# Performance work log

Measured on AMD Instinct MI355X. Metric: run time of the kernel, lower is better.

## Reference

```python
import jax, jax.numpy as jnp
import numpy as np

T, B, E, H = 1024, 2, 1024, 16
D = E // H


def setup_inputs() -> dict:
    key = jax.random.key(0)
    ks = jax.random.split(key, 5)
    s = 1.0 / np.sqrt(E)  # xavier_uniform bound ~ sqrt(6/(fan_in+fan_out)); scale suffices for a numeric baseline
    return {
        "query": jax.random.normal(ks[0], (T, B, E), jnp.float32),
        "key_": jax.random.normal(ks[1], (T, B, E), jnp.float32),
        "value": jax.random.normal(ks[2], (T, B, E), jnp.float32),
        "in_proj_weight": jax.random.uniform(ks[3], (3 * E, E), jnp.float32, -s, s),
        "in_proj_bias": jnp.zeros((3 * E,), jnp.float32),
        "out_proj_weight": jax.random.uniform(ks[4], (E, E), jnp.float32, -s, s),
        "out_proj_bias": jnp.zeros((E,), jnp.float32),
    }


def reference(query, key_, value, in_proj_weight, in_proj_bias, out_proj_weight, out_proj_bias):
    # Faithful to CumulativeLinearMultiheadAttentionKV.forward with
    # batch_first=False, is_causal=True, no padding mask, no kv cache.
    Tl, Bl, El = query.shape
    wq, wk, wv = jnp.split(in_proj_weight, 3, axis=0)
    bq, bk, bv = jnp.split(in_proj_bias, 3)
    q = query @ wq.T + bq          # (T, B, E)
    k = key_ @ wk.T + bk
    v = value @ wv.T + bv

    def to_bhtd(x):
        return x.reshape(Tl, Bl, H, D).transpose(1, 2, 0, 3)  # (B, H, T, D)

    q, k, v = to_bhtd(q), to_bhtd(k), to_bhtd(v)

    scale = 1.0 / np.sqrt(D)  # SDPA-style default scale (scale=None)
    # cumulative linear attention: prefix sums of k_s \otimes v_s
    kv = jnp.einsum('bhsk,bhsv->bhskv', k, v)        # (B, H, T, D, D)
    kv_store = jnp.cumsum(kv, axis=2)                # causal KV state per step
    out = jnp.einsum('bhtk,bhtkv->bhtv', q, kv_store) * scale  # (B, H, T, D)

    out = out.transpose(2, 0, 1, 3).reshape(Tl, Bl, El)  # back to (T, B, E)
    out = out @ out_proj_weight.T + out_proj_bias
    return out
```

## Files before the change

kernel.cpp:

```cpp
#include <hip/hip_runtime.h>


#define E_DIM 1024

typedef short bf16x8 __attribute__((ext_vector_type(8)));
typedef float f32x4  __attribute__((ext_vector_type(4)));

__device__ inline unsigned short f2bf(float f) {
    unsigned u = __builtin_bit_cast(unsigned, f);
    u = (u + 0x7FFFu + ((u >> 16) & 1u)) >> 16;
    return (unsigned short)u;
}

__device__ inline void gload_lds16(const void* g, void* l) {
    __builtin_amdgcn_global_load_lds(
        (const __attribute__((address_space(1))) unsigned int*)g,
        (__attribute__((address_space(3))) unsigned int*)l, 16, 0, 0);
}

__device__ inline int swzb(int row, int colbyte) {
    return colbyte ^ ((row & 7) << 4);
}

__global__ __launch_bounds__(256) void k_castw(
    const float* __restrict__ w_in, const float* __restrict__ w_out,
    unsigned short* __restrict__ dst)
{
    const int id8 = blockIdx.x * 256 + threadIdx.x;
    const int WI8 = 3 * E_DIM * E_DIM / 8;
    const float* src = (id8 < WI8) ? (w_in + (size_t)id8 * 8)
                                   : (w_out + (size_t)(id8 - WI8) * 8);
    float4 f0 = *reinterpret_cast<const float4*>(src);
    float4 f1 = *reinterpret_cast<const float4*>(src + 4);
    ushort4 o0, o1;
    o0.x = f2bf(f0.x); o0.y = f2bf(f0.y); o0.z = f2bf(f0.z); o0.w = f2bf(f0.w);
    o1.x = f2bf(f1.x); o1.y = f2bf(f1.y); o1.z = f2bf(f1.z); o1.w = f2bf(f1.w);
    *reinterpret_cast<ushort4*>(dst + (size_t)id8 * 8)     = o0;
    *reinterpret_cast<ushort4*>(dst + (size_t)id8 * 8 + 4) = o1;
}

__global__ __launch_bounds__(256) void k_gin(
    const float* __restrict__ q_in, const float* __restrict__ k_in,
    const float* __restrict__ v_in, const unsigned short* __restrict__ Wibf,
    const float* __restrict__ b_in,
    unsigned short* __restrict__ qslab, unsigned short* __restrict__ kslab,
    unsigned short* __restrict__ vtb)
{
    const int i = blockIdx.x;
    const int tile = (i & 7) * 48 + (i >> 3);
    const int z = tile >> 7;
    const int rem = tile & 127;
    const int x = rem >> 5, y = rem & 31;

    const float* X = (z == 0) ? q_in : (z == 1 ? k_in : v_in);
    const unsigned short* W = Wibf + (size_t)z * 1048576;
    const float* bz = b_in + z * E_DIM;

    const int nBase = x * 256;
    const int mBase = y * 64;
    const int b = mBase >> 10, tBase = mBase & 1023;

    __shared__ short As[2][64 * 64];
    __shared__ short Bs[2][256 * 64];

    const int tid = threadIdx.x;
    const int lane = tid & 63, wave = tid >> 6;
    const int wr = wave >> 1, wc = wave & 1;
    const int l15 = lane & 15, l4 = lane >> 4;

    auto stage = [&](int bufI, int k0) {
        #pragma unroll
        for (int l = 0; l < 8; ++l) {
            int off = l * 4096 + tid * 16;
            int row = off >> 7, cb = off & 127;
            gload_lds16((const char*)W + ((size_t)(nBase + row) * E_DIM + k0) * 2
                            + swzb(row, cb),
                        (char*)&Bs[bufI][0] + off);
        }
        #pragma unroll
        for (int l = 0; l < 2; ++l) {
            int u = tid + 256 * l;
            int row = u >> 3, cslot = u & 7;
            const float* src = &X[(size_t)((tBase + row) * 2 + b) * E_DIM
                                  + k0 + cslot * 8];
            float4 f0 = *reinterpret_cast<const float4*>(src);
            float4 f1 = *reinterpret_cast<const float4*>(src + 4);
            bf16x8 p;
            p[0] = (short)f2bf(f0.x); p[1] = (short)f2bf(f0.y);
            p[2] = (short)f2bf(f0.z); p[3] = (short)f2bf(f0.w);
            p[4] = (short)f2bf(f1.x); p[5] = (short)f2bf(f1.y);
            p[6] = (short)f2bf(f1.z); p[7] = (short)f2bf(f1.w);
            *reinterpret_cast<bf16x8*>(
                &As[bufI][row * 64 + (swzb(row, cslot * 16) >> 1)]) = p;
        }
    };

    f32x4 acc[2][8] = {};

    stage(0, 0);
    __syncthreads();
    int cur = 0;
    for (int it = 0; it < 16; ++it) {
        if (it < 15) stage(cur ^ 1, (it + 1) * 64);
        #pragma unroll
        for (int kk = 0; kk < 64; kk += 32) {
            bf16x8 af[2], bfr[8];
            #pragma unroll
            for (int ii = 0; ii < 2; ++ii) {
                int row = wr * 32 + ii * 16 + l15;
                af[ii] = *reinterpret_cast<const bf16x8*>(
                    &As[cur][row * 64 + (swzb(row, (kk + l4 * 8) * 2) >> 1)]);
            }
            #pragma unroll
            for (int j = 0; j < 8; ++j) {
                int row = wc * 128 + j * 16 + l15;
                bfr[j] = *reinterpret_cast<const bf16x8*>(
                    &Bs[cur][row * 64 + (swzb(row, (kk + l4 * 8) * 2) >> 1)]);
            }
            #pragma unroll
            for (int ii = 0; ii < 2; ++ii)
                #pragma unroll
                for (int j = 0; j < 8; ++j)
                    acc[ii][j] = __builtin_amdgcn_mfma_f32_16x16x32_bf16(
                        af[ii], bfr[j], acc[ii][j], 0, 0, 0);
        }
        __syncthreads();
        cur ^= 1;
    }

    #pragma unroll
    for (int ii = 0; ii < 2; ++ii) {
        int t0 = tBase + wr * 32 + ii * 16 + l4 * 4;
        #pragma unroll
        for (int j = 0; j < 8; ++j) {
            int col = nBase + wc * 128 + j * 16 + l15;
            float bv = bz[col];
            unsigned short v4[4];
            #pragma unroll
            for (int q = 0; q < 4; ++q) v4[q] = f2bf(acc[ii][j][q] + bv);
            if (z == 0) {
                #pragma unroll
                for (int q = 0; q < 4; ++q)
                    qslab[(size_t)b * 1048576 + (size_t)(t0 + q) * E_DIM + col] = v4[q];
            } else if (z == 1) {
                #pragma unroll
                for (int q = 0; q < 4; ++q)
                    kslab[(size_t)b * 1048576 + (size_t)(t0 + q) * E_DIM + col] = v4[q];
            } else {
                ushort4 w = {v4[0], v4[1], v4[2], v4[3]};
                *reinterpret_cast<ushort4*>(
                    &vtb[((size_t)b * 1024 + col) * 1024 + t0]) = w;
            }
        }
    }
}

__global__ __launch_bounds__(256) void k_attn(
    const unsigned short* __restrict__ qslab, const unsigned short* __restrict__ kslab,
    const unsigned short* __restrict__ vtb, unsigned short* __restrict__ attnbf)
{
    const int i = blockIdx.x;
    const int xcd = i & 7, u = i >> 3;
    const int bh = xcd * 4 + (u >> 4);
    const int qtr = u & 15;
    const int qt = ((u >> 5) & 1) ? (15 - qtr) : qtr;
    const int b = bh >> 4, h = bh & 15;
    const int colb = h * 64, t0q = qt * 64;

    __shared__ short Qs[64 * 64];
    __shared__ short Ks[2][64 * 64];
    __shared__ short Vts[2][64 * 64];
    __shared__ short Ss[64 * 72];

    const int tid = threadIdx.x;
    const int lane = tid & 63, wave = tid >> 6;
    const int wr = wave >> 1, wc = wave & 1;
    const int l15 = lane & 15, l4 = lane >> 4;

    auto stageKV = [&](int bufI, int c) {
        int t0k = c * 64;
        #pragma unroll
        for (int l = 0; l < 2; ++l) {
            int off = l * 4096 + tid * 16;
            int row = off >> 7, cb = off & 127;
            int scb = swzb(row, cb);
            gload_lds16((const char*)kslab +
                            ((size_t)b * 1048576 + (size_t)(t0k + row) * E_DIM + colb) * 2 + scb,
                        (char*)&Ks[bufI][0] + off);
            gload_lds16((const char*)vtb +
                            (((size_t)(b * 1024 + colb + row)) * 1024 + t0k) * 2 + scb,
                        (char*)&Vts[bufI][0] + off);
        }
    };

    #pragma unroll
    for (int l = 0; l < 2; ++l) {
        int off = l * 4096 + tid * 16;
        int row = off >> 7, cb = off & 127;
        gload_lds16((const char*)qslab +
                        ((size_t)b * 1048576 + (size_t)(t0q + row) * E_DIM + colb) * 2
                        + swzb(row, cb),
                    (char*)Qs + off);
    }
    stageKV(0, 0);
    __syncthreads();

    f32x4 oacc[2][2] = {};
    int cur = 0;

    for (int c = 0; c <= qt; ++c) {
        if (c < qt) stageKV(cur ^ 1, c + 1);

        f32x4 sacc[2][2] = {};
        #pragma unroll
        for (int kk = 0; kk < 64; kk += 32) {
            bf16x8 af[2], bfr[2];
            #pragma unroll
            for (int ii = 0; ii < 2; ++ii) {
                int row = wr * 32 + ii * 16 + l15;
                af[ii] = *reinterpret_cast<const bf16x8*>(
                    &Qs[row * 64 + (swzb(row, (kk + l4 * 8) * 2) >> 1)]);
            }
            #pragma unroll
            for (int j = 0; j < 2; ++j) {
                int row = wc * 32 + j * 16 + l15;
                bfr[j] = *reinterpret_cast<const bf16x8*>(
                    &Ks[cur][row * 64 + (swzb(row, (kk + l4 * 8) * 2) >> 1)]);
            }
            #pragma unroll
            for (int ii = 0; ii < 2; ++ii)
                #pragma unroll
                for (int j = 0; j < 2; ++j)
                    sacc[ii][j] = __builtin_amdgcn_mfma_f32_16x16x32_bf16(
                        af[ii], bfr[j], sacc[ii][j], 0, 0, 0);
        }
        const bool diag = (c == qt);
        #pragma unroll
        for (int ii = 0; ii < 2; ++ii) {
            #pragma unroll
            for (int j = 0; j < 2; ++j) {
                int kr = wc * 32 + j * 16 + l15;
                #pragma unroll
                for (int q = 0; q < 4; ++q) {
                    int qr = wr * 32 + ii * 16 + l4 * 4 + q;
                    short sv = (short)f2bf(sacc[ii][j][q]);
                    Ss[qr * 72 + kr] = (!diag || kr <= qr) ? sv : (short)0;
                }
            }
        }
        __syncthreads();

        #pragma unroll
        for (int kk = 0; kk < 64; kk += 32) {
            bf16x8 af[2], bfr[2];
            #pragma unroll
            for (int ii = 0; ii < 2; ++ii)
                af[ii] = *reinterpret_cast<const bf16x8*>(
                            &Ss[(wr * 32 + ii * 16 + l15) * 72 + kk + l4 * 8]);
            #pragma unroll
            for (int j = 0; j < 2; ++j) {
                int row = wc * 32 + j * 16 + l15;
                bfr[j] = *reinterpret_cast<const bf16x8*>(
                    &Vts[cur][row * 64 + (swzb(row, (kk + l4 * 8) * 2) >> 1)]);
            }
            #pragma unroll
            for (int ii = 0; ii < 2; ++ii)
                #pragma unroll
                for (int j = 0; j < 2; ++j)
                    oacc[ii][j] = __builtin_amdgcn_mfma_f32_16x16x32_bf16(
                        af[ii], bfr[j], oacc[ii][j], 0, 0, 0);
        }
        __syncthreads();
        cur ^= 1;
    }

    #pragma unroll
    for (int ii = 0; ii < 2; ++ii) {
        #pragma unroll
        for (int j = 0; j < 2; ++j) {
            int dv = wc * 32 + j * 16 + l15;
            #pragma unroll
            for (int q = 0; q < 4; ++q) {
                int qr = wr * 32 + ii * 16 + l4 * 4 + q;
                attnbf[(size_t)b * 1048576 + (size_t)(t0q + qr) * E_DIM + colb + dv] =
                    f2bf(oacc[ii][j][q] * 0.125f);
            }
        }
    }
}

__global__ __launch_bounds__(256) void k_gout(
    const unsigned short* __restrict__ attnbf, const unsigned short* __restrict__ Wobf,
    const float* __restrict__ bias, float* __restrict__ out)
{
    const int i = blockIdx.x;
    const int tile = (i & 7) * 64 + (i >> 3);
    const int x = tile & 15, y = tile >> 4;
    const int nBase = x * 64;
    const int mBase = y * 64;

    __shared__ short As[2][64 * 64];
    __shared__ short Bs[2][64 * 64];

    const int tid = threadIdx.x;
    const int lane = tid & 63, wave = tid >> 6;
    const int wr = wave >> 1, wc = wave & 1;
    const int l15 = lane & 15, l4 = lane >> 4;

    auto stage = [&](int bufI, int k0) {
        #pragma unroll
        for (int l = 0; l < 2; ++l) {
            int off = l * 4096 + tid * 16;
            int row = off >> 7, cb = off & 127;
            int scb = swzb(row, cb);
            gload_lds16((const char*)Wobf + ((size_t)(nBase + row) * E_DIM + k0) * 2 + scb,
                        (char*)&Bs[bufI][0] + off);
            int r = mBase + row, t = r >> 1, bb = r & 1;
            gload_lds16((const char*)attnbf +
                            ((size_t)bb * 1048576 + (size_t)t * E_DIM + k0) * 2 + scb,
                        (char*)&As[bufI][0] + off);
        }
    };

    f32x4 acc[2][2] = {};

    stage(0, 0);
    __syncthreads();
    int cur = 0;
    for (int it = 0; it < 16; ++it) {
        if (it < 15) stage(cur ^ 1, (it + 1) * 64);
        #pragma unroll
        for (int kk = 0; kk < 64; kk += 32) {
            bf16x8 af[2], bfr[2];
            #pragma unroll
            for (int ii = 0; ii < 2; ++ii) {
                int row = wr * 32 + ii * 16 + l15;
                af[ii] = *reinterpret_cast<const bf16x8*>(
                    &As[cur][row * 64 + (swzb(row, (kk + l4 * 8) * 2) >> 1)]);
            }
            #pragma unroll
            for (int j = 0; j < 2; ++j) {
                int row = wc * 32 + j * 16 + l15;
                bfr[j] = *reinterpret_cast<const bf16x8*>(
                    &Bs[cur][row * 64 + (swzb(row, (kk + l4 * 8) * 2) >> 1)]);
            }
            #pragma unroll
            for (int ii = 0; ii < 2; ++ii)
                #pragma unroll
                for (int j = 0; j < 2; ++j)
                    acc[ii][j] = __builtin_amdgcn_mfma_f32_16x16x32_bf16(
                        af[ii], bfr[j], acc[ii][j], 0, 0, 0);
        }
        __syncthreads();
        cur ^= 1;
    }

    #pragma unroll
    for (int ii = 0; ii < 2; ++ii) {
        int r0 = mBase + wr * 32 + ii * 16 + l4 * 4;
        #pragma unroll
        for (int j = 0; j < 2; ++j) {
            int col = nBase + wc * 32 + j * 16 + l15;
            float bv = bias[col];
            #pragma unroll
            for (int q = 0; q < 4; ++q)
                out[(size_t)(r0 + q) * E_DIM + col] = acc[ii][j][q] + bv;
        }
    }
}

extern "C" void kernel_launch(void* const* d_in, const int* in_sizes, int n_in,
                              void* d_out, int out_size, void* d_ws, size_t ws_size,
                              hipStream_t stream)
{
    const float* q_in  = (const float*)d_in[0];
    const float* k_in  = (const float*)d_in[1];
    const float* v_in  = (const float*)d_in[2];
    const float* w_in  = (const float*)d_in[3];
    const float* b_in  = (const float*)d_in[4];
    const float* w_out = (const float*)d_in[5];
    const float* b_out = (const float*)d_in[6];

    char* w = (char*)d_ws;
    unsigned short* Wibf   = (unsigned short*)w;
    unsigned short* Wobf   = (unsigned short*)(w + 6291456);
    unsigned short* qslab  = (unsigned short*)(w + 8388608);
    unsigned short* kslab  = (unsigned short*)(w + 12582912);
    unsigned short* vtb    = (unsigned short*)(w + 16777216);
    unsigned short* attnbf = (unsigned short*)(w + 20971520);
    float* outp = (float*)d_out;

    k_castw<<<2048, 256, 0, stream>>>(w_in, w_out, Wibf);
    k_gin<<<384, 256, 0, stream>>>(q_in, k_in, v_in, Wibf, b_in, qslab, kslab, vtb);
    k_attn<<<512, 256, 0, stream>>>(qslab, kslab, vtb, attnbf);
    k_gout<<<512, 256, 0, stream>>>(attnbf, Wobf, b_out, outp);
}
```

Baseline: 155.5 us.

## Accumulate K^T V prefix state for off-diagonal chunks instead of per-chunk QK^T

The attention kernel now builds a per-block prefix state P = sum over earlier chunks of K^T V, using a transposed K copy written by the input projection. It applies Q·P once and computes the masked QK^T·V only for the diagonal chunk. This removes the per-chunk S writes to LDS, the extra barrier and the second MFMA pass from the off-diagonal loop. In exchange, the projection writes an extra transposed K buffer, PTs adds LDS use, and P is rounded to bf16 before the final product, which may shift accuracy.

```diff
diff --git a/kernel.cpp b/kernel.cpp
--- a/kernel.cpp
+++ b/kernel.cpp
@@ -44,7 +44,7 @@
     const float* __restrict__ v_in, const unsigned short* __restrict__ Wibf,
     const float* __restrict__ b_in,
     unsigned short* __restrict__ qslab, unsigned short* __restrict__ kslab,
-    unsigned short* __restrict__ vtb)
+    unsigned short* __restrict__ ktb,   unsigned short* __restrict__ vtb)
 {
     const int i = blockIdx.x;
     const int tile = (i & 7) * 48 + (i >> 3);
@@ -146,6 +146,9 @@
                 #pragma unroll
                 for (int q = 0; q < 4; ++q)
                     kslab[(size_t)b * 1048576 + (size_t)(t0 + q) * E_DIM + col] = v4[q];
+                ushort4 w = {v4[0], v4[1], v4[2], v4[3]};
+                *reinterpret_cast<ushort4*>(
+                    &ktb[((size_t)b * 1024 + col) * 1024 + t0]) = w;
             } else {
                 ushort4 w = {v4[0], v4[1], v4[2], v4[3]};
                 *reinterpret_cast<ushort4*>(
@@ -157,7 +160,8 @@
 
 __global__ __launch_bounds__(256) void k_attn(
     const unsigned short* __restrict__ qslab, const unsigned short* __restrict__ kslab,
-    const unsigned short* __restrict__ vtb, unsigned short* __restrict__ attnbf)
+    const unsigned short* __restrict__ ktb,  const unsigned short* __restrict__ vtb,
+    unsigned short* __restrict__ attnbf)
 {
     const int i = blockIdx.x;
     const int xcd = i & 7, u = i >> 3;
@@ -168,28 +172,40 @@
     const int colb = h * 64, t0q = qt * 64;
 
     __shared__ short Qs[64 * 64];
-    __shared__ short Ks[2][64 * 64];
-    __shared__ short Vts[2][64 * 64];
+    __shared__ short KB[2][64 * 64];
+    __shared__ short VB[2][64 * 64];
     __shared__ short Ss[64 * 72];
+    __shared__ short PTs[64 * 72];
 
     const int tid = threadIdx.x;
     const int lane = tid & 63, wave = tid >> 6;
     const int wr = wave >> 1, wc = wave & 1;
     const int l15 = lane & 15, l4 = lane >> 4;
 
-    auto stageKV = [&](int bufI, int c) {
+    auto stageP = [&](int bufI, int c) {
         int t0k = c * 64;
+        #pragma unroll
+        for (int l = 0; l < 2; ++l) {
+            int off = l * 4096 + tid * 16;
+            int row = off >> 7, cb = off & 127;
+            int scb = swzb(row, cb);
+            size_t trn = ((size_t)(b * 1024 + colb + row)) * 1024 + t0k;
+            gload_lds16((const char*)ktb + trn * 2 + scb, (char*)&KB[bufI][0] + off);
+            gload_lds16((const char*)vtb + trn * 2 + scb, (char*)&VB[bufI][0] + off);
+        }
+    };
+    auto stageDiag = [&](int bufI) {
         #pragma unroll
         for (int l = 0; l < 2; ++l) {
             int off = l * 4096 + tid * 16;
             int row = off >> 7, cb = off & 127;
             int scb = swzb(row, cb);
             gload_lds16((const char*)kslab +
-                            ((size_t)b * 1048576 + (size_t)(t0k + row) * E_DIM + colb) * 2 + scb,
-                        (char*)&Ks[bufI][0] + off);
+                            ((size_t)b * 1048576 + (size_t)(t0q + row) * E_DIM + colb) * 2 + scb,
+                        (char*)&KB[bufI][0] + off);
             gload_lds16((const char*)vtb +
-                            (((size_t)(b * 1024 + colb + row)) * 1024 + t0k) * 2 + scb,
-                        (char*)&Vts[bufI][0] + off);
+                            (((size_t)(b * 1024 + colb + row)) * 1024 + t0q) * 2 + scb,
+                        (char*)&VB[bufI][0] + off);
         }
     };
 
@@ -202,16 +218,14 @@
                         + swzb(row, cb),
                     (char*)Qs + off);
     }
-    stageKV(0, 0);
+    if (qt > 0) stageP(0, 0); else stageDiag(0);
     __syncthreads();
 
-    f32x4 oacc[2][2] = {};
+    f32x4 pacc[2][2] = {};
     int cur = 0;
 
-    for (int c = 0; c <= qt; ++c) {
-        if (c < qt) stageKV(cur ^ 1, c + 1);
-
-        f32x4 sacc[2][2] = {};
+    for (int c = 0; c < qt; ++c) {
+        if (c + 1 < qt) stageP(cur ^ 1, c + 1); else stageDiag(cur ^ 1);
         #pragma unroll
         for (int kk = 0; kk < 64; kk += 32) {
             bf16x8 af[2], bfr[2];
@@ -219,59 +233,109 @@
             for (int ii = 0; ii < 2; ++ii) {
                 int row = wr * 32 + ii * 16 + l15;
                 af[ii] = *reinterpret_cast<const bf16x8*>(
-                    &Qs[row * 64 + (swzb(row, (kk + l4 * 8) * 2) >> 1)]);
+                    &KB[cur][row * 64 + (swzb(row, (kk + l4 * 8) * 2) >> 1)]);
             }
             #pragma unroll
             for (int j = 0; j < 2; ++j) {
                 int row = wc * 32 + j * 16 + l15;
                 bfr[j] = *reinterpret_cast<const bf16x8*>(
-                    &Ks[cur][row * 64 + (swzb(row, (kk + l4 * 8) * 2) >> 1)]);
+                    &VB[cur][row * 64 + (swzb(row, (kk + l4 * 8) * 2) >> 1)]);
             }
             #pragma unroll
             for (int ii = 0; ii < 2; ++ii)
                 #pragma unroll
                 for (int j = 0; j < 2; ++j)
-                    sacc[ii][j] = __builtin_amdgcn_mfma_f32_16x16x32_bf16(
-                        af[ii], bfr[j], sacc[ii][j], 0, 0, 0);
-        }
-        const bool diag = (c == qt);
-        #pragma unroll
-        for (int ii = 0; ii < 2; ++ii) {
-            #pragma unroll
-            for (int j = 0; j < 2; ++j) {
-                int kr = wc * 32 + j * 16 + l15;
-                #pragma unroll
-                for (int q = 0; q < 4; ++q) {
-                    int qr = wr * 32 + ii * 16 + l4 * 4 + q;
-                    short sv = (short)f2bf(sacc[ii][j][q]);
-                    Ss[qr * 72 + kr] = (!diag || kr <= qr) ? sv : (short)0;
-                }
-            }
-        }
-        __syncthreads();
-
-        #pragma unroll
-        for (int kk = 0; kk < 64; kk += 32) {
-            bf16x8 af[2], bfr[2];
-            #pragma unroll
-            for (int ii = 0; ii < 2; ++ii)
-                af[ii] = *reinterpret_cast<const bf16x8*>(
-                            &Ss[(wr * 32 + ii * 16 + l15) * 72 + kk + l4 * 8]);
-            #pragma unroll
-            for (int j = 0; j < 2; ++j) {
-                int row = wc * 32 + j * 16 + l15;
-                bfr[j] = *reinterpret_cast<const bf16x8*>(
-                    &Vts[cur][row * 64 + (swzb(row, (kk + l4 * 8) * 2) >> 1)]);
-            }
-            #pragma unroll
-            for (int ii = 0; ii < 2; ++ii)
-                #pragma unroll
-                for (int j = 0; j < 2; ++j)
-                    oacc[ii][j] = __builtin_amdgcn_mfma_f32_16x16x32_bf16(
-                        af[ii], bfr[j], oacc[ii][j], 0, 0, 0);
+                    pacc[ii][j] = __builtin_amdgcn_mfma_f32_16x16x32_bf16(
+                        af[ii], bfr[j], pacc[ii][j], 0, 0, 0);
         }
         __syncthreads();
         cur ^= 1;
+    }
+
+    f32x4 sacc[2][2] = {};
+    #pragma unroll
+    for (int kk = 0; kk < 64; kk += 32) {
+        bf16x8 af[2], bfr[2];
+        #pragma unroll
+        for (int ii = 0; ii < 2; ++ii) {
+            int row = wr * 32 + ii * 16 + l15;
+            af[ii] = *reinterpret_cast<const bf16x8*>(
+                &Qs[row * 64 + (swzb(row, (kk + l4 * 8) * 2) >> 1)]);
+        }
+        #pragma unroll
+        for (int j = 0; j < 2; ++j) {
+            int row = wc * 32 + j * 16 + l15;
+            bfr[j] = *reinterpret_cast<const bf16x8*>(
+                &KB[cur][row * 64 + (swzb(row, (kk + l4 * 8) * 2) >> 1)]);
+        }
+        #pragma unroll
+        for (int ii = 0; ii < 2; ++ii)
+            #pragma unroll
+            for (int j = 0; j < 2; ++j)
+                sacc[ii][j] = __builtin_amdgcn_mfma_f32_16x16x32_bf16(
+                    af[ii], bfr[j], sacc[ii][j], 0, 0, 0);
+    }
+
+    #pragma unroll
+    for (int ii = 0; ii < 2; ++ii) {
+        #pragma unroll
+        for (int j = 0; j < 2; ++j) {
+            int dv = wc * 32 + j * 16 + l15;
+            int dkb = wr * 32 + ii * 16 + l4 * 4;
+            ushort4 pw;
+            pw.x = f2bf(pacc[ii][j][0]); pw.y = f2bf(pacc[ii][j][1]);
+            pw.z = f2bf(pacc[ii][j][2]); pw.w = f2bf(pacc[ii][j][3]);
+            *reinterpret_cast<ushort4*>(&PTs[dv * 72 + dkb]) = pw;
+            int kr = dv;
+            #pragma unroll
+            for (int q = 0; q < 4; ++q) {
+                int qr = dkb + q;
+                Ss[qr * 72 + kr] = (kr <= qr) ? (short)f2bf(sacc[ii][j][q]) : (short)0;
+            }
+        }
+    }
+    __syncthreads();
+
+    f32x4 oacc[2][2] = {};
+    #pragma unroll
+    for (int kk = 0; kk < 64; kk += 32) {
+        bf16x8 af[2], bfr[2];
+        #pragma unroll
+        for (int ii = 0; ii < 2; ++ii)
+            af[ii] = *reinterpret_cast<const bf16x8*>(
+                        &Ss[(wr * 32 + ii * 16 + l15) * 72 + kk + l4 * 8]);
+        #pragma unroll
+        for (int j = 0; j < 2; ++j) {
+            int row = wc * 32 + j * 16 + l15;
+            bfr[j] = *reinterpret_cast<const bf16x8*>(
+                &VB[cur][row * 64 + (swzb(row, (kk + l4 * 8) * 2) >> 1)]);
+        }
+        #pragma unroll
+        for (int ii = 0; ii < 2; ++ii)
+            #pragma unroll
+            for (int j = 0; j < 2; ++j)
+                oacc[ii][j] = __builtin_amdgcn_mfma_f32_16x16x32_bf16(
+                    af[ii], bfr[j], oacc[ii][j], 0, 0, 0);
+    }
+    #pragma unroll
+    for (int kk = 0; kk < 64; kk += 32) {
+        bf16x8 af[2], bfr[2];
+        #pragma unroll
+        for (int ii = 0; ii < 2; ++ii) {
+            int row = wr * 32 + ii * 16 + l15;
+            af[ii] = *reinterpret_cast<const bf16x8*>(
+                &Qs[row * 64 + (swzb(row, (kk + l4 * 8) * 2) >> 1)]);
+        }
+        #pragma unroll
+        for (int j = 0; j < 2; ++j)
+            bfr[j] = *reinterpret_cast<const bf16x8*>(
+                        &PTs[(wc * 32 + j * 16 + l15) * 72 + kk + l4 * 8]);
+        #pragma unroll
+        for (int ii = 0; ii < 2; ++ii)
+            #pragma unroll
+            for (int j = 0; j < 2; ++j)
+                oacc[ii][j] = __builtin_amdgcn_mfma_f32_16x16x32_bf16(
+                    af[ii], bfr[j], oacc[ii][j], 0, 0, 0);
     }
 
     #pragma unroll
@@ -388,10 +452,12 @@
     unsigned short* kslab  = (unsigned short*)(w + 12582912);
     unsigned short* vtb    = (unsigned short*)(w + 16777216);
     unsigned short* attnbf = (unsigned short*)(w + 20971520);
+    unsigned short* ktb    = (unsigned short*)(w + 25165824);
     float* outp = (float*)d_out;
 
     k_castw<<<2048, 256, 0, stream>>>(w_in, w_out, Wibf);
-    k_gin<<<384, 256, 0, stream>>>(q_in, k_in, v_in, Wibf, b_in, qslab, kslab, vtb);
-    k_attn<<<512, 256, 0, stream>>>(qslab, kslab, vtb, attnbf);
+    k_gin<<<384, 256, 0, stream>>>(q_in, k_in, v_in, Wibf, b_in,
+                                   qslab, kslab, ktb, vtb);
+    k_attn<<<512, 256, 0, stream>>>(qslab, kslab, ktb, vtb, attnbf);
     k_gout<<<512, 256, 0, stream>>>(attnbf, Wobf, b_out, outp);
 }
```

Result: faster. 147.9 us (-4.9%).
